# Performance work log

Measured on AMD Instinct MI355X. Metric: run time of the kernel, lower is better.

Reference implementation:

```python
import math
import jax, jax.numpy as jnp
import numpy as np

D_MODEL = 2048
NUM_HEADS = 16
D_HEAD = D_MODEL // NUM_HEADS
THETA = 10000.0


def _rope_tables(seq_len, d_head):
    # interleaved-pair RoPE tables, shape (seq, d_head//2)
    idx = jnp.arange(0, d_head, 2, dtype=jnp.float32)
    inv_freq = THETA ** (-idx / d_head)
    angles = jnp.arange(seq_len, dtype=jnp.float32)[:, None] * inv_freq[None, :]
    return jnp.cos(angles), jnp.sin(angles)


def _apply_rope(x, cos, sin):
    # x: (B, H, S, d_head); cos/sin: (S, d_head//2)
    B, H, S, d = x.shape
    xp = x.reshape(B, H, S, d // 2, 2)
    xe, xo = xp[..., 0], xp[..., 1]
    rot = jnp.stack([xe * cos - xo * sin, xe * sin + xo * cos], axis=-1)
    return rot.reshape(B, H, S, d)


def setup_inputs() -> dict:
    key = jax.random.key(0)
    k_x, k_q, k_k, k_v, k_o = jax.random.split(key, 5)
    std = math.sqrt(2.0 / (D_MODEL + D_MODEL))
    x = jax.random.normal(k_x, (4, 2048, D_MODEL), dtype=jnp.float32)
    Wq = jax.random.normal(k_q, (D_MODEL, D_MODEL), dtype=jnp.float32) * std
    Wk = jax.random.normal(k_k, (D_MODEL, D_MODEL), dtype=jnp.float32) * std
    Wv = jax.random.normal(k_v, (D_MODEL, D_MODEL), dtype=jnp.float32) * std
    Wo = jax.random.normal(k_o, (D_MODEL, D_MODEL), dtype=jnp.float32) * std
    return {"x": x, "Wq": Wq, "Wk": Wk, "Wv": Wv, "Wo": Wo}


def reference(x, Wq, Wk, Wv, Wo):
    B, S, D = x.shape
    H, dh = NUM_HEADS, D_HEAD
    # projections: weight stored (out, in), y = x @ W^T
    def proj(W):
        y = jnp.einsum('bsi,oi->bso', x, W)
        return y.reshape(B, S, H, dh).transpose(0, 2, 1, 3)  # (B,H,S,dh)
    q, k, v = proj(Wq), proj(Wk), proj(Wv)

    cos, sin = _rope_tables(S, dh)
    q = _apply_rope(q, cos, sin)
    k = _apply_rope(k, cos, sin)

    # naive fp32 attention with causal mask
    scores = jnp.einsum('bhqd,bhkd->bhqk', q.astype(jnp.float32), k.astype(jnp.float32)) / math.sqrt(dh)
    causal = jnp.tril(jnp.ones((S, S), dtype=bool))
    scores = jnp.where(causal, scores, jnp.finfo(jnp.float32).min)
    probs = jax.nn.softmax(scores, axis=-1).astype(v.dtype)
    attn = jnp.einsum('bhqk,bhkd->bhqd', probs, v)

    attn = attn.transpose(0, 2, 1, 3).reshape(B, S, D)
    return jnp.einsum('bsi,oi->bso', attn, Wo)
```

## Files before the change

### kernel.cpp

```cpp
#include <hip/hip_runtime.h>

typedef float f32x4 __attribute__((ext_vector_type(4)));
typedef _Float16 f16x8 __attribute__((ext_vector_type(8)));
typedef unsigned short u16x8 __attribute__((ext_vector_type(8)));
typedef unsigned short u16x4 __attribute__((ext_vector_type(4)));

#define KD 2048

static __device__ __forceinline__ unsigned short f2h(float f) {
    _Float16 h = (_Float16)f;
    return __builtin_bit_cast(unsigned short, h);
}
static __device__ __forceinline__ float h2f(unsigned short u) {
    return (float)__builtin_bit_cast(_Float16, u);
}
static __device__ __forceinline__ void gl16(const unsigned short* g, unsigned short* l) {
    __builtin_amdgcn_global_load_lds(
        (const __attribute__((address_space(1))) unsigned int*)g,
        (__attribute__((address_space(3))) unsigned int*)l, 16, 0, 0);
}

__global__ void rope_tables(float* __restrict__ cosT, float* __restrict__ sinT) {
    int i = blockIdx.x * 256 + threadIdx.x;
    if (i >= 2048 * 64) return;
    int s = i >> 6, j = i & 63;
    float freq = exp2f(-(2.0f * (float)j / 128.0f) * 13.287712379549449f);
    float a = (float)s * freq;
    cosT[i] = cosf(a);
    sinT[i] = sinf(a);
}

__global__ void precvt(const float* __restrict__ src, unsigned short* __restrict__ dst, int n4) {
    int i = blockIdx.x * 256 + threadIdx.x;
    if (i >= n4) return;
    f32x4 v = ((const f32x4*)src)[i];
    u16x4 h = { f2h(v[0]), f2h(v[1]), f2h(v[2]), f2h(v[3]) };
    ((u16x4*)dst)[i] = h;
}
__global__ void precvtW(const float* __restrict__ s0, const float* __restrict__ s1,
                        const float* __restrict__ s2, const float* __restrict__ s3,
                        unsigned short* __restrict__ d0, unsigned short* __restrict__ d1,
                        unsigned short* __restrict__ d2, unsigned short* __restrict__ d3) {
    int i = blockIdx.x * 256 + threadIdx.x;
    if (i >= 1048576) return;
    const float* s = blockIdx.y == 0 ? s0 : blockIdx.y == 1 ? s1 : blockIdx.y == 2 ? s2 : s3;
    unsigned short* d = blockIdx.y == 0 ? d0 : blockIdx.y == 1 ? d1 : blockIdx.y == 2 ? d2 : d3;
    f32x4 v = ((const f32x4*)s)[i];
    u16x4 h = { f2h(v[0]), f2h(v[1]), f2h(v[2]), f2h(v[3]) };
    ((u16x4*)d)[i] = h;
}

template<int MODE>
__global__ __launch_bounds__(256)
void gemm4(const unsigned short* __restrict__ Ah, const unsigned short* __restrict__ Bh,
           void* __restrict__ OutH,
           const float* __restrict__ cosT, const float* __restrict__ sinT)
{
    const int bi = blockIdx.x, bj = blockIdx.y;
    const int tid = threadIdx.x;
    const int lane = tid & 63;
    const int w = tid >> 6;
    const int wm = w >> 1, wn = w & 1;
    const int lg = lane >> 4, lr = lane & 15;

    __shared__ unsigned short As[2][128 * 32];
    __shared__ unsigned short Bs[2][128 * 32];

    f32x4 acc[4][4];
#pragma unroll
    for (int i = 0; i < 4; ++i)
#pragma unroll
        for (int j = 0; j < 4; ++j) acc[i][j] = f32x4{0.f, 0.f, 0.f, 0.f};

    const int srow = lane >> 2;
    const int schk = (lane & 3) ^ ((lane >> 4) & 3);

    auto stage = [&](int k0, int buf) {
#pragma unroll
        for (int q2 = 0; q2 < 2; ++q2) {
            const int seg = w * 2 + q2;
            const int row = seg * 16 + srow;
            const int loff = seg * 512 + lane * 8;
            const size_t ga = (size_t)(bi * 128 + row) * KD + k0 + schk * 8;
            const size_t gb = (size_t)(bj * 128 + row) * KD + k0 + schk * 8;
            gl16(Ah + ga, &As[buf][loff]);
            gl16(Bh + gb, &Bs[buf][loff]);
        }
    };
    const int roff = 8 * (lg ^ ((lr >> 2) & 3));
    auto term = [&](const unsigned short* A_, const unsigned short* B_) {
        const unsigned short* Ap = A_ + (wm * 64 + lr) * 32;
        const unsigned short* Bp = B_ + (wn * 64 + lr) * 32;
        f16x8 af[4], bf[4];
#pragma unroll
        for (int i = 0; i < 4; ++i) {
            af[i] = *(const f16x8*)(Ap + i * 512 + roff);
            bf[i] = *(const f16x8*)(Bp + i * 512 + roff);
        }
#pragma unroll
        for (int mi = 0; mi < 4; ++mi)
#pragma unroll
            for (int ni = 0; ni < 4; ++ni)
                acc[mi][ni] = __builtin_amdgcn_mfma_f32_16x16x32_f16(af[mi], bf[ni], acc[mi][ni], 0, 0, 0);
    };

    stage(0, 0);
#pragma unroll 1
    for (int kt = 0; kt < 64; ++kt) {
        const int cur = kt & 1;
        __syncthreads();
        if (kt < 63) stage((kt + 1) * 32, cur ^ 1);
        term(As[cur], Bs[cur]);
    }

    if constexpr (MODE <= 1) {
        unsigned short* OH = (unsigned short*)OutH;
        const float scale = (MODE == 0) ? 0.08838834764831845f : 1.0f;
#pragma unroll
        for (int mi = 0; mi < 4; ++mi) {
            int i0 = bi * 128 + wm * 64 + mi * 16 + lg * 4;
            int h = i0 >> 7, dd = i0 & 127;
            int jp = dd >> 1;
#pragma unroll
            for (int ni = 0; ni < 4; ++ni) {
                int jj = bj * 128 + wn * 64 + ni * 16 + lr;
                int b = jj >> 11, s = jj & 2047;
                float c0 = cosT[s * 64 + jp],     s0 = sinT[s * 64 + jp];
                float c1 = cosT[s * 64 + jp + 1], s1 = sinT[s * 64 + jp + 1];
                f32x4 v = acc[mi][ni];
                float r0 = (v[0] * c0 - v[1] * s0) * scale;
                float r1 = (v[0] * s0 + v[1] * c0) * scale;
                float r2 = (v[2] * c1 - v[3] * s1) * scale;
                float r3 = (v[2] * s1 + v[3] * c1) * scale;
                u16x4 ph = { f2h(r0), f2h(r1), f2h(r2), f2h(r3) };
                *(u16x4*)&OH[((size_t)(b * 16 + h) * 2048 + s) * 128 + dd] = ph;
            }
        }
    } else if constexpr (MODE == 2) {
        unsigned short* O = (unsigned short*)OutH;
#pragma unroll
        for (int mi = 0; mi < 4; ++mi) {
            int i0 = bi * 128 + wm * 64 + mi * 16 + lg * 4;
            int b = i0 >> 11, s = i0 & 2047;
#pragma unroll
            for (int ni = 0; ni < 4; ++ni) {
                int jj = bj * 128 + wn * 64 + ni * 16 + lr;
                int h = jj >> 7, dd = jj & 127;
                f32x4 v = acc[mi][ni];
                u16x4 pk = { f2h(v[0]), f2h(v[1]), f2h(v[2]), f2h(v[3]) };
                *(u16x4*)&O[((size_t)(b * 16 + h) * 128 + dd) * 2048 + s] = pk;
            }
        }
    } else {
        float* O = (float*)OutH;
#pragma unroll
        for (int mi = 0; mi < 4; ++mi) {
            int i0 = bi * 128 + wm * 64 + mi * 16 + lg * 4;
#pragma unroll
            for (int ni = 0; ni < 4; ++ni) {
                int jj = bj * 128 + wn * 64 + ni * 16 + lr;
                *(f32x4*)&O[(size_t)jj * 2048 + i0] = acc[mi][ni];
            }
        }
    }
}

__global__ __launch_bounds__(256)
void attn6(const unsigned short* __restrict__ Qh, const unsigned short* __restrict__ Kh,
           const unsigned short* __restrict__ Vt, unsigned short* __restrict__ Ob)
{
    const int bid = blockIdx.x;
    const int bh = bid & 63;
    const int p  = bid >> 6;
    const int tid = threadIdx.x;
    const int lane = tid & 63, w = tid >> 6;
    const int lg = lane >> 4, lr = lane & 15;
    const int b = bh >> 4, h = bh & 15;

    __shared__ unsigned short Ks[2][32 * 128];
    __shared__ unsigned short Vs[2][128 * 32];
    __shared__ unsigned short Ps[4][16 * 40];

    auto stage = [&](int t) {
        const int buf = t & 1;
        const int kv0 = t * 32;
#pragma unroll
        for (int q2 = 0; q2 < 2; ++q2) {
            const int seg = w * 2 + q2;
            {
                const int row = seg * 4 + (lane >> 4);
                const int gcol = 8 * ((lane & 15) ^ (row & 7));
                gl16(Kh + ((size_t)bh * 2048 + kv0 + row) * 128 + gcol,
                     &Ks[buf][seg * 512 + lane * 8]);
            }
            {
                const int row = seg * 16 + (lane >> 2);
                const int gcol = 8 * ((lane & 3) ^ ((row >> 1) & 3));
                gl16(Vt + ((size_t)bh * 128 + row) * 2048 + kv0 + gcol,
                     &Vs[buf][seg * 512 + lane * 8]);
            }
        }
    };

#pragma unroll 1
    for (int half = 0; half < 2; ++half) {
        const int qt = half ? p : (15 - p);
        const int qbase = qt * 128 + w * 32;
        const int qmaxw = qbase + 31;
        const int nkv = 4 * (qt + 1);

        f16x8 qf[2][4];
#pragma unroll
        for (int qg = 0; qg < 2; ++qg) {
            const size_t qoff = ((size_t)bh * 2048 + qbase + qg * 16 + lr) * 128;
#pragma unroll
            for (int kk = 0; kk < 4; ++kk)
                qf[qg][kk] = *(const f16x8*)(Qh + qoff + kk * 32 + lg * 8);
        }

        f32x4 o[8][2];
#pragma unroll
        for (int i = 0; i < 8; ++i)
#pragma unroll
            for (int qg = 0; qg < 2; ++qg) o[i][qg] = f32x4{0.f, 0.f, 0.f, 0.f};
        float m_run[2] = { -1e30f, -1e30f }, l_run[2] = { 0.f, 0.f };

        stage(0);
        __syncthreads();

#pragma unroll 1
        for (int t = 0; t < nkv; ++t) {
            if (t + 1 < nkv) stage(t + 1);
            const int buf = t & 1;
            const int kv0 = t * 32;
            if (kv0 <= qmaxw) {
                f32x4 sc[2][2];
#pragma unroll
                for (int m2 = 0; m2 < 2; ++m2)
#pragma unroll
                    for (int qg = 0; qg < 2; ++qg) sc[m2][qg] = f32x4{0.f, 0.f, 0.f, 0.f};
#pragma unroll
                for (int m2 = 0; m2 < 2; ++m2)
#pragma unroll
                    for (int kk = 0; kk < 4; ++kk) {
                        const int go = 8 * ((4 * kk + lg) ^ (lr & 7));
                        f16x8 kf = *(const f16x8*)&Ks[buf][(m2 * 16 + lr) * 128 + go];
#pragma unroll
                        for (int qg = 0; qg < 2; ++qg)
                            sc[m2][qg] = __builtin_amdgcn_mfma_f32_16x16x32_f16(kf, qf[qg][kk], sc[m2][qg], 0, 0, 0);
                    }
#pragma unroll
                for (int qg = 0; qg < 2; ++qg) {
                    const int q = qbase + qg * 16 + lr;
                    float pmax = -1e30f;
#pragma unroll
                    for (int m2 = 0; m2 < 2; ++m2)
#pragma unroll
                        for (int rr = 0; rr < 4; ++rr) {
                            int kvg = kv0 + m2 * 16 + lg * 4 + rr;
                            float sv = (kvg <= q) ? sc[m2][qg][rr] : -1e30f;
                            sc[m2][qg][rr] = sv;
                            pmax = fmaxf(pmax, sv);
                        }
                    pmax = fmaxf(pmax, __shfl_xor(pmax, 16));
                    pmax = fmaxf(pmax, __shfl_xor(pmax, 32));
                    if (!__all(pmax <= m_run[qg] + 8.0f)) {
                        float mnew = fmaxf(m_run[qg], pmax);
                        float alpha = __expf(m_run[qg] - mnew);
                        m_run[qg] = mnew;
                        l_run[qg] *= alpha;
#pragma unroll
                        for (int ni = 0; ni < 8; ++ni) {
                            o[ni][qg][0] *= alpha; o[ni][qg][1] *= alpha;
                            o[ni][qg][2] *= alpha; o[ni][qg][3] *= alpha;
                        }
                    }
                    float psum = 0.f;
                    u16x4 pq[2];
#pragma unroll
                    for (int m2 = 0; m2 < 2; ++m2)
#pragma unroll
                        for (int rr = 0; rr < 4; ++rr) {
                            float pv = __expf(sc[m2][qg][rr] - m_run[qg]);
                            unsigned short ph = f2h(pv);
                            pq[m2][rr] = ph;
                            psum += h2f(ph);
                        }
                    l_run[qg] += psum;
                    *(u16x4*)&Ps[w][lr * 40 + lg * 4]      = pq[0];
                    *(u16x4*)&Ps[w][lr * 40 + 16 + lg * 4] = pq[1];
                    f16x8 pf = *(const f16x8*)&Ps[w][lr * 40 + lg * 8];
#pragma unroll
                    for (int ni = 0; ni < 8; ++ni) {
                        f16x8 vf = *(const f16x8*)&Vs[buf][(ni * 16 + lr) * 32 + 8 * (lg ^ ((lr >> 1) & 3))];
                        o[ni][qg] = __builtin_amdgcn_mfma_f32_16x16x32_f16(vf, pf, o[ni][qg], 0, 0, 0);
                    }
                }
            }
            __syncthreads();
        }

#pragma unroll
        for (int qg = 0; qg < 2; ++qg) {
            float l = l_run[qg];
            l += __shfl_xor(l, 16);
            l += __shfl_xor(l, 32);
            float inv = 1.f / l;
            const int q = qbase + qg * 16 + lr;
            unsigned short* Op = Ob + (((size_t)(b * 2048 + q) * 16 + h) * 128);
#pragma unroll
            for (int ni = 0; ni < 8; ++ni) {
                u16x4 pk = { f2h(o[ni][qg][0] * inv), f2h(o[ni][qg][1] * inv),
                             f2h(o[ni][qg][2] * inv), f2h(o[ni][qg][3] * inv) };
                *(u16x4*)&Op[ni * 16 + lg * 4] = pk;
            }
        }
    }
}

extern "C" void kernel_launch(void* const* d_in, const int* in_sizes, int n_in,
                              void* d_out, int out_size, void* d_ws, size_t ws_size,
                              hipStream_t stream) {
    const float* x  = (const float*)d_in[0];
    const float* Wq = (const float*)d_in[1];
    const float* Wk = (const float*)d_in[2];
    const float* Wv = (const float*)d_in[3];
    const float* Wo = (const float*)d_in[4];

    char* ws = (char*)d_ws;
    float* cosT = (float*)ws;
    float* sinT = cosT + 2048 * 64;
    unsigned short* xh  = (unsigned short*)(ws + (1 << 20));
    unsigned short* Vt  = xh  + (size_t)16777216;
    unsigned short* Wqh = Vt  + (size_t)16777216;
    unsigned short* Wkh = Wqh + (size_t)4194304;
    unsigned short* Wvh = Wkh + (size_t)4194304;
    unsigned short* Woh = Wvh + (size_t)4194304;

    unsigned short* attn_b = xh;

    unsigned short* Qh = (unsigned short*)d_out;
    unsigned short* Kh = Qh + (size_t)16777216;

    rope_tables<<<dim3(512), 256, 0, stream>>>(cosT, sinT);
    precvt<<<dim3(16384), 256, 0, stream>>>(x, xh, 4194304);
    precvtW<<<dim3(4096, 4), 256, 0, stream>>>(Wq, Wk, Wv, Wo, Wqh, Wkh, Wvh, Woh);

    gemm4<0><<<dim3(16, 64), 256, 0, stream>>>(Wqh, xh, Qh, cosT, sinT);
    gemm4<1><<<dim3(16, 64), 256, 0, stream>>>(Wkh, xh, Kh, cosT, sinT);
    gemm4<2><<<dim3(64, 16), 256, 0, stream>>>(xh, Wvh, Vt, cosT, sinT);
    attn6<<<dim3(512), 256, 0, stream>>>(Qh, Kh, Vt, attn_b);
    gemm4<3><<<dim3(16, 64), 256, 0, stream>>>(Woh, attn_b, d_out, cosT, sinT);
}
```

Measured before the change: 571.8 us.

## Merge QKV GEMMs and conversions into single launches, shrink attention q-tiles

Folds the x and weight fp16 conversions into one kernel and runs the Q, K and V projections as one grid of 3072 blocks, cutting launches and tail effects between dependent kernels. Attention now processes 64-query tiles with 16 queries per wave over 1024 blocks for more parallelism and a finer causal split. Its softmax switches to exp2 with log2e folded into the Q scale, and masking is applied only on the diagonal tile. It also sums unrounded probabilities. The trade-off is less K/V reuse per loaded tile, and the runtime mode branch in the GEMM epilogue adds some register pressure.

Result: slower. 588.2 us (+2.9%).

```diff
diff --git a/kernel.cpp b/kernel.cpp
--- a/kernel.cpp
+++ b/kernel.cpp
@@ -10,9 +10,6 @@
 static __device__ __forceinline__ unsigned short f2h(float f) {
     _Float16 h = (_Float16)f;
     return __builtin_bit_cast(unsigned short, h);
-}
-static __device__ __forceinline__ float h2f(unsigned short u) {
-    return (float)__builtin_bit_cast(_Float16, u);
 }
 static __device__ __forceinline__ void gl16(const unsigned short* g, unsigned short* l) {
     __builtin_amdgcn_global_load_lds(
@@ -30,33 +27,41 @@
     sinT[i] = sinf(a);
 }
 
-__global__ void precvt(const float* __restrict__ src, unsigned short* __restrict__ dst, int n4) {
+__global__ void precvt_all(const float* __restrict__ x,
+                           const float* __restrict__ Wq, const float* __restrict__ Wk,
+                           const float* __restrict__ Wv, const float* __restrict__ Wo,
+                           unsigned short* __restrict__ xh,
+                           unsigned short* __restrict__ Wqh, unsigned short* __restrict__ Wkh,
+                           unsigned short* __restrict__ Wvh, unsigned short* __restrict__ Woh) {
     int i = blockIdx.x * 256 + threadIdx.x;
-    if (i >= n4) return;
-    f32x4 v = ((const f32x4*)src)[i];
+    const float* s; unsigned short* d; int off;
+    if (i < 4194304) { s = x; d = xh; off = i; }
+    else {
+        int j = i - 4194304; int m = j >> 20; off = j & 1048575;
+        s = m == 0 ? Wq : m == 1 ? Wk : m == 2 ? Wv : Wo;
+        d = m == 0 ? Wqh : m == 1 ? Wkh : m == 2 ? Wvh : Woh;
+    }
+    f32x4 v = ((const f32x4*)s)[off];
     u16x4 h = { f2h(v[0]), f2h(v[1]), f2h(v[2]), f2h(v[3]) };
-    ((u16x4*)dst)[i] = h;
-}
-__global__ void precvtW(const float* __restrict__ s0, const float* __restrict__ s1,
-                        const float* __restrict__ s2, const float* __restrict__ s3,
-                        unsigned short* __restrict__ d0, unsigned short* __restrict__ d1,
-                        unsigned short* __restrict__ d2, unsigned short* __restrict__ d3) {
-    int i = blockIdx.x * 256 + threadIdx.x;
-    if (i >= 1048576) return;
-    const float* s = blockIdx.y == 0 ? s0 : blockIdx.y == 1 ? s1 : blockIdx.y == 2 ? s2 : s3;
-    unsigned short* d = blockIdx.y == 0 ? d0 : blockIdx.y == 1 ? d1 : blockIdx.y == 2 ? d2 : d3;
-    f32x4 v = ((const f32x4*)s)[i];
-    u16x4 h = { f2h(v[0]), f2h(v[1]), f2h(v[2]), f2h(v[3]) };
-    ((u16x4*)d)[i] = h;
-}
-
-template<int MODE>
+    ((u16x4*)d)[off] = h;
+}
+
 __global__ __launch_bounds__(256)
-void gemm4(const unsigned short* __restrict__ Ah, const unsigned short* __restrict__ Bh,
-           void* __restrict__ OutH,
-           const float* __restrict__ cosT, const float* __restrict__ sinT)
+void gemm_qkv(const unsigned short* __restrict__ xh,
+              const unsigned short* __restrict__ Wqh, const unsigned short* __restrict__ Wkh,
+              const unsigned short* __restrict__ Wvh,
+              unsigned short* __restrict__ Qh, unsigned short* __restrict__ Kh,
+              unsigned short* __restrict__ Vt,
+              const float* __restrict__ cosT, const float* __restrict__ sinT)
 {
-    const int bi = blockIdx.x, bj = blockIdx.y;
+    const int bid = blockIdx.x;
+    const int mode = bid >> 10;
+    const int r = bid & 1023;
+    int bi, bj;
+    const unsigned short *Ah, *Bh;
+    if (mode <= 1) { bi = r >> 6; bj = r & 63; Ah = mode ? Wkh : Wqh; Bh = xh; }
+    else           { bi = r >> 4; bj = r & 15; Ah = xh;              Bh = Wvh; }
+
     const int tid = threadIdx.x;
     const int lane = tid & 63;
     const int w = tid >> 6;
@@ -113,9 +118,9 @@
         term(As[cur], Bs[cur]);
     }
 
-    if constexpr (MODE <= 1) {
-        unsigned short* OH = (unsigned short*)OutH;
-        const float scale = (MODE == 0) ? 0.08838834764831845f : 1.0f;
+    if (mode <= 1) {
+        unsigned short* OH = mode ? Kh : Qh;
+        const float scale = mode ? 1.0f : 0.12751743343f;
 #pragma unroll
         for (int mi = 0; mi < 4; ++mi) {
             int i0 = bi * 128 + wm * 64 + mi * 16 + lg * 4;
@@ -136,8 +141,7 @@
                 *(u16x4*)&OH[((size_t)(b * 16 + h) * 2048 + s) * 128 + dd] = ph;
             }
         }
-    } else if constexpr (MODE == 2) {
-        unsigned short* O = (unsigned short*)OutH;
+    } else {
 #pragma unroll
         for (int mi = 0; mi < 4; ++mi) {
             int i0 = bi * 128 + wm * 64 + mi * 16 + lg * 4;
@@ -148,25 +152,86 @@
                 int h = jj >> 7, dd = jj & 127;
                 f32x4 v = acc[mi][ni];
                 u16x4 pk = { f2h(v[0]), f2h(v[1]), f2h(v[2]), f2h(v[3]) };
-                *(u16x4*)&O[((size_t)(b * 16 + h) * 128 + dd) * 2048 + s] = pk;
+                *(u16x4*)&Vt[((size_t)(b * 16 + h) * 128 + dd) * 2048 + s] = pk;
             }
         }
-    } else {
-        float* O = (float*)OutH;
-#pragma unroll
-        for (int mi = 0; mi < 4; ++mi) {
-            int i0 = bi * 128 + wm * 64 + mi * 16 + lg * 4;
-#pragma unroll
-            for (int ni = 0; ni < 4; ++ni) {
-                int jj = bj * 128 + wn * 64 + ni * 16 + lr;
-                *(f32x4*)&O[(size_t)jj * 2048 + i0] = acc[mi][ni];
-            }
-        }
     }
 }
 
 __global__ __launch_bounds__(256)
-void attn6(const unsigned short* __restrict__ Qh, const unsigned short* __restrict__ Kh,
+void gemm_o(const unsigned short* __restrict__ Ah, const unsigned short* __restrict__ Bh,
+            float* __restrict__ O)
+{
+    const int bi = blockIdx.x, bj = blockIdx.y;
+    const int tid = threadIdx.x;
+    const int lane = tid & 63;
+    const int w = tid >> 6;
+    const int wm = w >> 1, wn = w & 1;
+    const int lg = lane >> 4, lr = lane & 15;
+
+    __shared__ unsigned short As[2][128 * 32];
+    __shared__ unsigned short Bs[2][128 * 32];
+
+    f32x4 acc[4][4];
+#pragma unroll
+    for (int i = 0; i < 4; ++i)
+#pragma unroll
+        for (int j = 0; j < 4; ++j) acc[i][j] = f32x4{0.f, 0.f, 0.f, 0.f};
+
+    const int srow = lane >> 2;
+    const int schk = (lane & 3) ^ ((lane >> 4) & 3);
+
+    auto stage = [&](int k0, int buf) {
+#pragma unroll
+        for (int q2 = 0; q2 < 2; ++q2) {
+            const int seg = w * 2 + q2;
+            const int row = seg * 16 + srow;
+            const int loff = seg * 512 + lane * 8;
+            const size_t ga = (size_t)(bi * 128 + row) * KD + k0 + schk * 8;
+            const size_t gb = (size_t)(bj * 128 + row) * KD + k0 + schk * 8;
+            gl16(Ah + ga, &As[buf][loff]);
+            gl16(Bh + gb, &Bs[buf][loff]);
+        }
+    };
+    const int roff = 8 * (lg ^ ((lr >> 2) & 3));
+    auto term = [&](const unsigned short* A_, const unsigned short* B_) {
+        const unsigned short* Ap = A_ + (wm * 64 + lr) * 32;
+        const unsigned short* Bp = B_ + (wn * 64 + lr) * 32;
+        f16x8 af[4], bf[4];
+#pragma unroll
+        for (int i = 0; i < 4; ++i) {
+            af[i] = *(const f16x8*)(Ap + i * 512 + roff);
+            bf[i] = *(const f16x8*)(Bp + i * 512 + roff);
+        }
+#pragma unroll
+        for (int mi = 0; mi < 4; ++mi)
+#pragma unroll
+            for (int ni = 0; ni < 4; ++ni)
+                acc[mi][ni] = __builtin_amdgcn_mfma_f32_16x16x32_f16(af[mi], bf[ni], acc[mi][ni], 0, 0, 0);
+    };
+
+    stage(0, 0);
+#pragma unroll 1
+    for (int kt = 0; kt < 64; ++kt) {
+        const int cur = kt & 1;
+        __syncthreads();
+        if (kt < 63) stage((kt + 1) * 32, cur ^ 1);
+        term(As[cur], Bs[cur]);
+    }
+
+#pragma unroll
+    for (int mi = 0; mi < 4; ++mi) {
+        int i0 = bi * 128 + wm * 64 + mi * 16 + lg * 4;
+#pragma unroll
+        for (int ni = 0; ni < 4; ++ni) {
+            int jj = bj * 128 + wn * 64 + ni * 16 + lr;
+            *(f32x4*)&O[(size_t)jj * 2048 + i0] = acc[mi][ni];
+        }
+    }
+}
+
+__global__ __launch_bounds__(256)
+void attn7(const unsigned short* __restrict__ Qh, const unsigned short* __restrict__ Kh,
            const unsigned short* __restrict__ Vt, unsigned short* __restrict__ Ob)
 {
     const int bid = blockIdx.x;
@@ -204,26 +269,24 @@
 
 #pragma unroll 1
     for (int half = 0; half < 2; ++half) {
-        const int qt = half ? p : (15 - p);
-        const int qbase = qt * 128 + w * 32;
-        const int qmaxw = qbase + 31;
-        const int nkv = 4 * (qt + 1);
-
-        f16x8 qf[2][4];
-#pragma unroll
-        for (int qg = 0; qg < 2; ++qg) {
-            const size_t qoff = ((size_t)bh * 2048 + qbase + qg * 16 + lr) * 128;
+        const int qt = half ? p : (31 - p);
+        const int qbase = qt * 64 + w * 16;
+        const int q = qbase + lr;
+        const int t_last = (qbase + 15) >> 5;
+        const int nkv = 2 * (qt + 1);
+
+        f16x8 qf[4];
+        {
+            const size_t qoff = ((size_t)bh * 2048 + q) * 128;
 #pragma unroll
             for (int kk = 0; kk < 4; ++kk)
-                qf[qg][kk] = *(const f16x8*)(Qh + qoff + kk * 32 + lg * 8);
-        }
-
-        f32x4 o[8][2];
-#pragma unroll
-        for (int i = 0; i < 8; ++i)
-#pragma unroll
-            for (int qg = 0; qg < 2; ++qg) o[i][qg] = f32x4{0.f, 0.f, 0.f, 0.f};
-        float m_run[2] = { -1e30f, -1e30f }, l_run[2] = { 0.f, 0.f };
+                qf[kk] = *(const f16x8*)(Qh + qoff + kk * 32 + lg * 8);
+        }
+
+        f32x4 o[8];
+#pragma unroll
+        for (int i = 0; i < 8; ++i) o[i] = f32x4{0.f, 0.f, 0.f, 0.f};
+        float m_run = -1e30f, l_run = 0.f;
 
         stage(0);
         __syncthreads();
@@ -232,88 +295,74 @@
         for (int t = 0; t < nkv; ++t) {
             if (t + 1 < nkv) stage(t + 1);
             const int buf = t & 1;
-            const int kv0 = t * 32;
-            if (kv0 <= qmaxw) {
-                f32x4 sc[2][2];
-#pragma unroll
-                for (int m2 = 0; m2 < 2; ++m2)
-#pragma unroll
-                    for (int qg = 0; qg < 2; ++qg) sc[m2][qg] = f32x4{0.f, 0.f, 0.f, 0.f};
+            if (t <= t_last) {
+                f32x4 sc[2] = { f32x4{0.f,0.f,0.f,0.f}, f32x4{0.f,0.f,0.f,0.f} };
 #pragma unroll
                 for (int m2 = 0; m2 < 2; ++m2)
 #pragma unroll
                     for (int kk = 0; kk < 4; ++kk) {
                         const int go = 8 * ((4 * kk + lg) ^ (lr & 7));
                         f16x8 kf = *(const f16x8*)&Ks[buf][(m2 * 16 + lr) * 128 + go];
-#pragma unroll
-                        for (int qg = 0; qg < 2; ++qg)
-                            sc[m2][qg] = __builtin_amdgcn_mfma_f32_16x16x32_f16(kf, qf[qg][kk], sc[m2][qg], 0, 0, 0);
+                        sc[m2] = __builtin_amdgcn_mfma_f32_16x16x32_f16(kf, qf[kk], sc[m2], 0, 0, 0);
                     }
-#pragma unroll
-                for (int qg = 0; qg < 2; ++qg) {
-                    const int q = qbase + qg * 16 + lr;
-                    float pmax = -1e30f;
+                if (t == t_last) {
+                    const int kv0 = t * 32;
 #pragma unroll
                     for (int m2 = 0; m2 < 2; ++m2)
 #pragma unroll
                         for (int rr = 0; rr < 4; ++rr) {
                             int kvg = kv0 + m2 * 16 + lg * 4 + rr;
-                            float sv = (kvg <= q) ? sc[m2][qg][rr] : -1e30f;
-                            sc[m2][qg][rr] = sv;
-                            pmax = fmaxf(pmax, sv);
+                            if (kvg > q) sc[m2][rr] = -1e30f;
                         }
-                    pmax = fmaxf(pmax, __shfl_xor(pmax, 16));
-                    pmax = fmaxf(pmax, __shfl_xor(pmax, 32));
-                    if (!__all(pmax <= m_run[qg] + 8.0f)) {
-                        float mnew = fmaxf(m_run[qg], pmax);
-                        float alpha = __expf(m_run[qg] - mnew);
-                        m_run[qg] = mnew;
-                        l_run[qg] *= alpha;
-#pragma unroll
-                        for (int ni = 0; ni < 8; ++ni) {
-                            o[ni][qg][0] *= alpha; o[ni][qg][1] *= alpha;
-                            o[ni][qg][2] *= alpha; o[ni][qg][3] *= alpha;
-                        }
+                }
+                float pmax = fmaxf(fmaxf(fmaxf(sc[0][0], sc[0][1]), fmaxf(sc[0][2], sc[0][3])),
+                                   fmaxf(fmaxf(sc[1][0], sc[1][1]), fmaxf(sc[1][2], sc[1][3])));
+                pmax = fmaxf(pmax, __shfl_xor(pmax, 16));
+                pmax = fmaxf(pmax, __shfl_xor(pmax, 32));
+                if (!__all(pmax <= m_run + 11.54f)) {
+                    float mnew = fmaxf(m_run, pmax);
+                    float alpha = exp2f(m_run - mnew);
+                    m_run = mnew;
+                    l_run *= alpha;
+#pragma unroll
+                    for (int ni = 0; ni < 8; ++ni) {
+                        o[ni][0] *= alpha; o[ni][1] *= alpha;
+                        o[ni][2] *= alpha; o[ni][3] *= alpha;
                     }
-                    float psum = 0.f;
-                    u16x4 pq[2];
-#pragma unroll
-                    for (int m2 = 0; m2 < 2; ++m2)
-#pragma unroll
-                        for (int rr = 0; rr < 4; ++rr) {
-                            float pv = __expf(sc[m2][qg][rr] - m_run[qg]);
-                            unsigned short ph = f2h(pv);
-                            pq[m2][rr] = ph;
-                            psum += h2f(ph);
-                        }
-                    l_run[qg] += psum;
-                    *(u16x4*)&Ps[w][lr * 40 + lg * 4]      = pq[0];
-                    *(u16x4*)&Ps[w][lr * 40 + 16 + lg * 4] = pq[1];
-                    f16x8 pf = *(const f16x8*)&Ps[w][lr * 40 + lg * 8];
-#pragma unroll
-                    for (int ni = 0; ni < 8; ++ni) {
-                        f16x8 vf = *(const f16x8*)&Vs[buf][(ni * 16 + lr) * 32 + 8 * (lg ^ ((lr >> 1) & 3))];
-                        o[ni][qg] = __builtin_amdgcn_mfma_f32_16x16x32_f16(vf, pf, o[ni][qg], 0, 0, 0);
+                }
+                float psum = 0.f;
+                u16x4 pq[2];
+#pragma unroll
+                for (int m2 = 0; m2 < 2; ++m2)
+#pragma unroll
+                    for (int rr = 0; rr < 4; ++rr) {
+                        float pv = exp2f(sc[m2][rr] - m_run);
+                        psum += pv;
+                        pq[m2][rr] = f2h(pv);
                     }
+                l_run += psum;
+                *(u16x4*)&Ps[w][lr * 40 + lg * 4]      = pq[0];
+                *(u16x4*)&Ps[w][lr * 40 + 16 + lg * 4] = pq[1];
+                f16x8 pf = *(const f16x8*)&Ps[w][lr * 40 + lg * 8];
+#pragma unroll
+                for (int ni = 0; ni < 8; ++ni) {
+                    f16x8 vf = *(const f16x8*)&Vs[buf][(ni * 16 + lr) * 32 + 8 * (lg ^ ((lr >> 1) & 3))];
+                    o[ni] = __builtin_amdgcn_mfma_f32_16x16x32_f16(vf, pf, o[ni], 0, 0, 0);
                 }
             }
             __syncthreads();
         }
 
-#pragma unroll
-        for (int qg = 0; qg < 2; ++qg) {
-            float l = l_run[qg];
-            l += __shfl_xor(l, 16);
-            l += __shfl_xor(l, 32);
-            float inv = 1.f / l;
-            const int q = qbase + qg * 16 + lr;
-            unsigned short* Op = Ob + (((size_t)(b * 2048 + q) * 16 + h) * 128);
-#pragma unroll
-            for (int ni = 0; ni < 8; ++ni) {
-                u16x4 pk = { f2h(o[ni][qg][0] * inv), f2h(o[ni][qg][1] * inv),
-                             f2h(o[ni][qg][2] * inv), f2h(o[ni][qg][3] * inv) };
-                *(u16x4*)&Op[ni * 16 + lg * 4] = pk;
-            }
+        float l = l_run;
+        l += __shfl_xor(l, 16);
+        l += __shfl_xor(l, 32);
+        float inv = 1.f / l;
+        unsigned short* Op = Ob + (((size_t)(b * 2048 + q) * 16 + h) * 128);
+#pragma unroll
+        for (int ni = 0; ni < 8; ++ni) {
+            u16x4 pk = { f2h(o[ni][0] * inv), f2h(o[ni][1] * inv),
+                         f2h(o[ni][2] * inv), f2h(o[ni][3] * inv) };
+            *(u16x4*)&Op[ni * 16 + lg * 4] = pk;
         }
     }
 }
@@ -343,12 +392,9 @@
     unsigned short* Kh = Qh + (size_t)16777216;
 
     rope_tables<<<dim3(512), 256, 0, stream>>>(cosT, sinT);
-    precvt<<<dim3(16384), 256, 0, stream>>>(x, xh, 4194304);
-    precvtW<<<dim3(4096, 4), 256, 0, stream>>>(Wq, Wk, Wv, Wo, Wqh, Wkh, Wvh, Woh);
-
-    gemm4<0><<<dim3(16, 64), 256, 0, stream>>>(Wqh, xh, Qh, cosT, sinT);
-    gemm4<1><<<dim3(16, 64), 256, 0, stream>>>(Wkh, xh, Kh, cosT, sinT);
-    gemm4<2><<<dim3(64, 16), 256, 0, stream>>>(xh, Wvh, Vt, cosT, sinT);
-    attn6<<<dim3(512), 256, 0, stream>>>(Qh, Kh, Vt, attn_b);
-    gemm4<3><<<dim3(16, 64), 256, 0, stream>>>(Woh, attn_b, d_out, cosT, sinT);
-}
+    precvt_all<<<dim3(32768), 256, 0, stream>>>(x, Wq, Wk, Wv, Wo,
+                                                xh, Wqh, Wkh, Wvh, Woh);
+    gemm_qkv<<<dim3(3072), 256, 0, stream>>>(xh, Wqh, Wkh, Wvh, Qh, Kh, Vt, cosT, sinT);
+    attn7<<<dim3(1024), 256, 0, stream>>>(Qh, Kh, Vt, attn_b);
+    gemm_o<<<dim3(16, 64), 256, 0, stream>>>(Woh, attn_b, (float*)d_out);
+}
```
